# Kernel optimization log

Hardware: AMD Instinct MI355X
Metric: run time of the kernel (lower is better)

The kernel has to match this reference:

```python
import jax, jax.numpy as jnp
import numpy as np

EPS = 1e-5
PATCH_SIZES = [None, 13]
PATCH_WEIGHTS = [0.5, 0.5]


def _box(x, p):
    # sliding-window sum over spatial dims, VALID padding -> [B,C,H-p+1,W-p+1]
    return jax.lax.reduce_window(x, 0.0, jax.lax.add, (1, 1, p, p), (1, 1, 1, 1), 'VALID')


def _global_ncc(x1, x2):
    # InstanceNorm2d (biased var, eps) per (b,c) over spatial dims, then dot / (c*h*w)
    b, c, h, w = x1.shape
    m1 = jnp.mean(x1, axis=(2, 3), keepdims=True)
    m2 = jnp.mean(x2, axis=(2, 3), keepdims=True)
    v1 = jnp.mean((x1 - m1) ** 2, axis=(2, 3), keepdims=True)
    v2 = jnp.mean((x2 - m2) ** 2, axis=(2, 3), keepdims=True)
    n1 = (x1 - m1) * jax.lax.rsqrt(v1 + EPS)
    n2 = (x2 - m2) * jax.lax.rsqrt(v2 + EPS)
    return jnp.sum(n1 * n2, axis=(1, 2, 3)) / (c * h * w)


def _patch_ncc(x1, x2, p):
    # Equivalent fused form of: unfold -> rearrange (patch locations become
    # channels, pxp patch pixels become spatial) -> InstanceNorm2d -> dot.
    # Each pxp patch is normalized over its own pixels => local NCC.
    b, c, h, w = x1.shape
    n = p * p
    s1 = _box(x1, p)
    s2 = _box(x2, p)
    s11 = _box(x1 * x1, p)
    s22 = _box(x2 * x2, p)
    s12 = _box(x1 * x2, p)
    m1 = s1 / n
    m2 = s2 / n
    v1 = s11 / n - m1 * m1  # biased variance, matches InstanceNorm2d
    v2 = s22 / n - m2 * m2
    cross = s12 - n * m1 * m2  # sum_p (I-mI)(J-mJ)
    cc = cross * jax.lax.rsqrt((v1 + EPS) * (v2 + EPS))  # [B,C,H',W']
    hp, wp = h - p + 1, w - p + 1
    # original divides by (channels' * h' * w') where channels' = c*hp*wp, spatial = p*p
    return jnp.sum(cc, axis=(1, 2, 3)) / (c * hp * wp * n)


def setup_inputs() -> dict:
    key = jax.random.key(0)
    k1, k2 = jax.random.split(key)
    x1 = jax.random.normal(k1, (32, 1, 512, 512), dtype=jnp.float32)
    x2 = jax.random.normal(k2, (32, 1, 512, 512), dtype=jnp.float32)
    return {"x1": x1, "x2": x2}


def reference(x1, x2):
    scores = []
    for w, p in zip(PATCH_WEIGHTS, PATCH_SIZES):
        if p is None:
            scores.append(w * _global_ncc(x1, x2))
        else:
            scores.append(w * _patch_ncc(x1, x2, p))
    return jnp.stack(scores, axis=0).sum(axis=0)  # [B]
```

## Files before the change

kernel.cpp:

```cpp
#include <hip/hip_runtime.h>

#define EPS 1e-5f

typedef float v2f __attribute__((ext_vector_type(2)));

constexpr int B = 32;
constexpr int H = 512;
constexpr int W = 512;
constexpr int NPIX = H * W;
constexpr int P = 13;
constexpr int HP = H - P + 1;
constexpr int WP = W - P + 1;
constexpr int TILES_X = 4;
constexpr int BAND_OUT = 40;
constexpr int BANDS_Y = 13;
constexpr int G = 13;
constexpr int NGROUPS = 4;
constexpr int ITER_LAST_OWN = 20;
constexpr int ITER_LAST_EMIT = 32;
constexpr int BLOCKS_PER_B = TILES_X * BANDS_Y;
constexpr int RS = 140;

#define GLOAD_LDS16(gp, lp)                                                    \
  __builtin_amdgcn_global_load_lds(                                            \
      (const __attribute__((address_space(1))) unsigned int*)(const void*)(gp),\
      (__attribute__((address_space(3))) unsigned int*)(void*)(lp), 16, 0, 0)

__global__ __launch_bounds__(64) void ncc_fused_kernel(
    const float* __restrict__ x1, const float* __restrict__ x2,
    float* __restrict__ part) {
  const int bid = blockIdx.x;
  const int b    = bid / BLOCKS_PER_B;
  const int rem  = bid % BLOCKS_PER_B;
  const int tile = rem % TILES_X;
  const int band = rem / TILES_X;
  const bool last = (band == BANDS_Y - 1);
  const int x0 = tile * 128;
  const int y0 = last ? (HP - BAND_OUT) : band * BAND_OUT;
  const int tid = threadIdx.x;
  const int c0 = x0 + 2 * tid;
  const bool valid0 = c0 < WP;
  const bool valid1 = (c0 + 1) < WP;

  __shared__ float sa[2][G][RS];
  __shared__ float sb[2][G][RS];

  const float* r1 = x1 + (size_t)b * NPIX + (size_t)y0 * W + x0;
  const float* r2 = x2 + (size_t)b * NPIX + (size_t)y0 * W + x0;

  int qoff = tid * 4;
  { int mx = W - x0 - 4; if (qoff > mx) qoff = mx; }
  const bool loader = tid < 35;

  auto stage = [&](int g, int buf) {
    if (loader) {
#pragma unroll
      for (int r = 0; r < G; ++r) {
        GLOAD_LDS16(r1 + (size_t)(g * G + r) * W + qoff, &sa[buf][r][0]);
        GLOAD_LDS16(r2 + (size_t)(g * G + r) * W + qoff, &sb[buf][r][0]);
      }
    }
  };

  v2f rr1[G], rr2[G], rr11[G], rr22[G], rr12[G];
  v2f S1 = {0.f, 0.f}, S2 = {0.f, 0.f}, S11 = {0.f, 0.f}, S22 = {0.f, 0.f},
      S12 = {0.f, 0.f};
  v2f g1 = {0.f, 0.f}, g2 = {0.f, 0.f}, g11 = {0.f, 0.f}, g22 = {0.f, 0.f},
      g12 = {0.f, 0.f};
  float acc = 0.f;
  const float inv_n = 1.0f / 169.0f;

  auto step = [&](int u, int buf, int t, bool fill) {
    const float* pa = &sa[buf][u][2 * tid];
    const float* pb = &sb[buf][u][2 * tid];
    v2f A[7], Bv[7];
#pragma unroll
    for (int k = 0; k < 7; ++k) {
      A[k] = *(const v2f*)(pa + 2 * k);
      Bv[k] = *(const v2f*)(pb + 2 * k);
    }

    v2f q11 = A[0] * A[0], q22 = Bv[0] * Bv[0], q12 = A[0] * Bv[0];
    v2f h1v = A[0], h2v = Bv[0], h11v = q11, h22v = q22, h12v = q12;
#pragma unroll
    for (int k = 1; k < 6; ++k) {
      h1v += A[k];
      h2v += Bv[k];
      h11v += A[k] * A[k];
      h22v += Bv[k] * Bv[k];
      h12v += A[k] * Bv[k];
    }
    float a12 = A[6].x, b12 = Bv[6].x, a13 = A[6].y, b13 = Bv[6].y;
    float h1_0 = h1v.x + h1v.y + a12;
    float h2_0 = h2v.x + h2v.y + b12;
    float h11_0 = fmaf(a12, a12, h11v.x + h11v.y);
    float h22_0 = fmaf(b12, b12, h22v.x + h22v.y);
    float h12_0 = fmaf(a12, b12, h12v.x + h12v.y);
    v2f h1 = {h1_0, h1_0 - A[0].x + a13};
    v2f h2 = {h2_0, h2_0 - Bv[0].x + b13};
    v2f h11 = {h11_0, fmaf(a13, a13, h11_0 - q11.x)};
    v2f h22 = {h22_0, fmaf(b13, b13, h22_0 - q22.x)};
    v2f h12 = {h12_0, fmaf(a13, b13, h12_0 - q12.x)};

    bool owned = last ? (t >= ITER_LAST_OWN) : (t < BAND_OUT);
    if (owned) {
      g1 += A[0]; g2 += Bv[0]; g11 += q11; g22 += q22; g12 += q12;
    }

    if (fill) {
      S1 += h1; S2 += h2; S11 += h11; S22 += h22; S12 += h12;
    } else {
      S1 += h1 - rr1[u]; S2 += h2 - rr2[u];
      S11 += h11 - rr11[u]; S22 += h22 - rr22[u]; S12 += h12 - rr12[u];
    }
    rr1[u] = h1; rr2[u] = h2; rr11[u] = h11; rr22[u] = h22; rr12[u] = h12;

    bool do_out = (t >= 12) && (!last || t >= ITER_LAST_EMIT);
    if (do_out) {
      v2f m1 = S1 * inv_n, m2 = S2 * inv_n;
      v2f vv1 = S11 * inv_n - m1 * m1 + EPS;
      v2f vv2 = S22 * inv_n - m2 * m2 + EPS;
      v2f cross = S12 - (S1 * inv_n) * S2;
      v2f den = vv1 * vv2;
      float cc0 = cross.x * rsqrtf(den.x);
      float cc1 = cross.y * rsqrtf(den.y);
      acc += (valid0 ? cc0 : 0.f) + (valid1 ? cc1 : 0.f);
    }
  };

  stage(0, 0);
  __syncthreads();
  stage(1, 1);

#pragma unroll
  for (int u = 0; u < G; ++u) step(u, 0, u, true);
  __syncthreads();

#pragma clang loop unroll(disable)
  for (int g = 1; g < NGROUPS; ++g) {
    if (g + 1 < NGROUPS) stage(g + 1, (g + 1) & 1);
    const int buf = g & 1;
#pragma unroll
    for (int u = 0; u < G; ++u) step(u, buf, g * G + u, false);
    __syncthreads();
  }

  float v0 = acc;
  float w1 = g1.x + g1.y, w2 = g2.x + g2.y;
  float w3 = g11.x + g11.y, w4 = g22.x + g22.y, w5 = g12.x + g12.y;
#pragma unroll
  for (int off = 32; off > 0; off >>= 1) {
    v0 += __shfl_down(v0, off, 64);
    w1 += __shfl_down(w1, off, 64);
    w2 += __shfl_down(w2, off, 64);
    w3 += __shfl_down(w3, off, 64);
    w4 += __shfl_down(w4, off, 64);
    w5 += __shfl_down(w5, off, 64);
  }
  if (tid == 0) {
    float* o = part + (size_t)bid * 6;
    o[0] = v0; o[1] = w1; o[2] = w2; o[3] = w3; o[4] = w4; o[5] = w5;
  }
}

__global__ __launch_bounds__(64) void final_kernel(
    const float* __restrict__ part, float* __restrict__ out) {
  int b = blockIdx.x;
  int tid = threadIdx.x;
  float s[6] = {0.f, 0.f, 0.f, 0.f, 0.f, 0.f};
  for (int i = tid; i < BLOCKS_PER_B; i += 64) {
    const float* p = part + (size_t)(b * BLOCKS_PER_B + i) * 6;
#pragma unroll
    for (int k = 0; k < 6; ++k) s[k] += p[k];
  }
#pragma unroll
  for (int off = 32; off > 0; off >>= 1) {
#pragma unroll
    for (int k = 0; k < 6; ++k) s[k] += __shfl_down(s[k], off, 64);
  }
  if (tid == 0) {
    float Nf = (float)NPIX;
    float m1 = s[1] / Nf;
    float m2 = s[2] / Nf;
    float v1 = fmaf(-m1, m1, s[3] / Nf);
    float v2 = fmaf(-m2, m2, s[4] / Nf);
    float cross = fmaf(-Nf * m1, m2, s[5]);
    float g = cross * rsqrtf((v1 + EPS) * (v2 + EPS)) / Nf;
    float patch = s[0] / ((float)HP * (float)WP * 169.0f);
    out[b] = 0.5f * g + 0.5f * patch;
  }
}

extern "C" void kernel_launch(void* const* d_in, const int* in_sizes, int n_in,
                              void* d_out, int out_size, void* d_ws, size_t ws_size,
                              hipStream_t stream) {
  const float* x1 = (const float*)d_in[0];
  const float* x2 = (const float*)d_in[1];
  float* out = (float*)d_out;
  float* part = (float*)d_ws;

  ncc_fused_kernel<<<B * BLOCKS_PER_B, 64, 0, stream>>>(x1, x2, part);
  final_kernel<<<B, 64, 0, stream>>>(part, out);
}
```

Baseline: 122.3 us.

## Add fp16 conversion prepass with global stats; run patch kernel on fp16 inputs

```diff
diff --git a/kernel.cpp b/kernel.cpp
--- a/kernel.cpp
+++ b/kernel.cpp
@@ -3,6 +3,8 @@
 #define EPS 1e-5f
 
 typedef float v2f __attribute__((ext_vector_type(2)));
+typedef _Float16 h2 __attribute__((ext_vector_type(2)));
+typedef _Float16 h4 __attribute__((ext_vector_type(4)));
 
 constexpr int B = 32;
 constexpr int H = 512;
@@ -16,18 +18,63 @@
 constexpr int BANDS_Y = 13;
 constexpr int G = 13;
 constexpr int NGROUPS = 4;
-constexpr int ITER_LAST_OWN = 20;
 constexpr int ITER_LAST_EMIT = 32;
 constexpr int BLOCKS_PER_B = TILES_X * BANDS_Y;
-constexpr int RS = 140;
+constexpr int RSH = 144;
 
 #define GLOAD_LDS16(gp, lp)                                                    \
   __builtin_amdgcn_global_load_lds(                                            \
       (const __attribute__((address_space(1))) unsigned int*)(const void*)(gp),\
       (__attribute__((address_space(3))) unsigned int*)(void*)(lp), 16, 0, 0)
 
+__global__ __launch_bounds__(256) void prepass_kernel(
+    const float* __restrict__ x1, const float* __restrict__ x2,
+    _Float16* __restrict__ p1, _Float16* __restrict__ p2,
+    float* __restrict__ gs) {
+  int b = blockIdx.x >> 5;
+  int chunk = blockIdx.x & 31;
+  int tid = threadIdx.x;
+  size_t base4 = (size_t)b * (NPIX / 4) + (size_t)chunk * 2048;
+  const float4* q1 = (const float4*)x1 + base4;
+  const float4* q2 = (const float4*)x2 + base4;
+  h4* o1 = (h4*)p1 + base4;
+  h4* o2 = (h4*)p2 + base4;
+
+  float s1 = 0.f, s2 = 0.f, s11 = 0.f, s22 = 0.f, s12 = 0.f;
+#pragma unroll
+  for (int i = 0; i < 8; ++i) {
+    float4 a = q1[i * 256 + tid];
+    float4 c = q2[i * 256 + tid];
+    s1 += a.x + a.y + a.z + a.w;
+    s2 += c.x + c.y + c.z + c.w;
+    s11 = fmaf(a.x, a.x, fmaf(a.y, a.y, fmaf(a.z, a.z, fmaf(a.w, a.w, s11))));
+    s22 = fmaf(c.x, c.x, fmaf(c.y, c.y, fmaf(c.z, c.z, fmaf(c.w, c.w, s22))));
+    s12 = fmaf(a.x, c.x, fmaf(a.y, c.y, fmaf(a.z, c.z, fmaf(a.w, c.w, s12))));
+    h4 ha = {(_Float16)a.x, (_Float16)a.y, (_Float16)a.z, (_Float16)a.w};
+    h4 hc = {(_Float16)c.x, (_Float16)c.y, (_Float16)c.z, (_Float16)c.w};
+    o1[i * 256 + tid] = ha;
+    o2[i * 256 + tid] = hc;
+  }
+
+  float v[5] = {s1, s2, s11, s22, s12};
+  __shared__ float red[5][4];
+#pragma unroll
+  for (int k = 0; k < 5; ++k)
+#pragma unroll
+    for (int off = 32; off > 0; off >>= 1) v[k] += __shfl_down(v[k], off, 64);
+  int lane = tid & 63, wave = tid >> 6;
+  if (lane == 0)
+#pragma unroll
+    for (int k = 0; k < 5; ++k) red[k][wave] = v[k];
+  __syncthreads();
+  if (tid == 0)
+#pragma unroll
+    for (int k = 0; k < 5; ++k)
+      atomicAdd(&gs[k * B + b], red[k][0] + red[k][1] + red[k][2] + red[k][3]);
+}
+
 __global__ __launch_bounds__(64) void ncc_fused_kernel(
-    const float* __restrict__ x1, const float* __restrict__ x2,
+    const _Float16* __restrict__ p1, const _Float16* __restrict__ p2,
     float* __restrict__ part) {
   const int bid = blockIdx.x;
   const int b    = bid / BLOCKS_PER_B;
@@ -42,15 +89,15 @@
   const bool valid0 = c0 < WP;
   const bool valid1 = (c0 + 1) < WP;
 
-  __shared__ float sa[2][G][RS];
-  __shared__ float sb[2][G][RS];
-
-  const float* r1 = x1 + (size_t)b * NPIX + (size_t)y0 * W + x0;
-  const float* r2 = x2 + (size_t)b * NPIX + (size_t)y0 * W + x0;
-
-  int qoff = tid * 4;
-  { int mx = W - x0 - 4; if (qoff > mx) qoff = mx; }
-  const bool loader = tid < 35;
+  __shared__ _Float16 sa[2][G][RSH];
+  __shared__ _Float16 sb[2][G][RSH];
+
+  const _Float16* r1 = p1 + (size_t)b * NPIX + (size_t)y0 * W + x0;
+  const _Float16* r2 = p2 + (size_t)b * NPIX + (size_t)y0 * W + x0;
+
+  int qoff = tid * 8;
+  { int mx = W - x0 - 8; if (qoff > mx) qoff = mx; }
+  const bool loader = tid < 18;
 
   auto stage = [&](int g, int buf) {
     if (loader) {
@@ -65,19 +112,19 @@
   v2f rr1[G], rr2[G], rr11[G], rr22[G], rr12[G];
   v2f S1 = {0.f, 0.f}, S2 = {0.f, 0.f}, S11 = {0.f, 0.f}, S22 = {0.f, 0.f},
       S12 = {0.f, 0.f};
-  v2f g1 = {0.f, 0.f}, g2 = {0.f, 0.f}, g11 = {0.f, 0.f}, g22 = {0.f, 0.f},
-      g12 = {0.f, 0.f};
   float acc = 0.f;
   const float inv_n = 1.0f / 169.0f;
 
   auto step = [&](int u, int buf, int t, bool fill) {
-    const float* pa = &sa[buf][u][2 * tid];
-    const float* pb = &sb[buf][u][2 * tid];
+    const h2* pa = (const h2*)&sa[buf][u][0];
+    const h2* pb = (const h2*)&sb[buf][u][0];
     v2f A[7], Bv[7];
 #pragma unroll
     for (int k = 0; k < 7; ++k) {
-      A[k] = *(const v2f*)(pa + 2 * k);
-      Bv[k] = *(const v2f*)(pb + 2 * k);
+      h2 xa = pa[tid + k];
+      h2 xb = pb[tid + k];
+      A[k].x = (float)xa.x;  A[k].y = (float)xa.y;
+      Bv[k].x = (float)xb.x; Bv[k].y = (float)xb.y;
     }
 
     v2f q11 = A[0] * A[0], q22 = Bv[0] * Bv[0], q12 = A[0] * Bv[0];
@@ -102,11 +149,6 @@
     v2f h22 = {h22_0, fmaf(b13, b13, h22_0 - q22.x)};
     v2f h12 = {h12_0, fmaf(a13, b13, h12_0 - q12.x)};
 
-    bool owned = last ? (t >= ITER_LAST_OWN) : (t < BAND_OUT);
-    if (owned) {
-      g1 += A[0]; g2 += Bv[0]; g11 += q11; g22 += q22; g12 += q12;
-    }
-
     if (fill) {
       S1 += h1; S2 += h2; S11 += h11; S22 += h22; S12 += h12;
     } else {
@@ -145,48 +187,29 @@
     __syncthreads();
   }
 
-  float v0 = acc;
-  float w1 = g1.x + g1.y, w2 = g2.x + g2.y;
-  float w3 = g11.x + g11.y, w4 = g22.x + g22.y, w5 = g12.x + g12.y;
-#pragma unroll
-  for (int off = 32; off > 0; off >>= 1) {
-    v0 += __shfl_down(v0, off, 64);
-    w1 += __shfl_down(w1, off, 64);
-    w2 += __shfl_down(w2, off, 64);
-    w3 += __shfl_down(w3, off, 64);
-    w4 += __shfl_down(w4, off, 64);
-    w5 += __shfl_down(w5, off, 64);
-  }
-  if (tid == 0) {
-    float* o = part + (size_t)bid * 6;
-    o[0] = v0; o[1] = w1; o[2] = w2; o[3] = w3; o[4] = w4; o[5] = w5;
-  }
+#pragma unroll
+  for (int off = 32; off > 0; off >>= 1) acc += __shfl_down(acc, off, 64);
+  if (tid == 0) part[bid] = acc;
 }
 
 __global__ __launch_bounds__(64) void final_kernel(
-    const float* __restrict__ part, float* __restrict__ out) {
+    const float* __restrict__ part, const float* __restrict__ gs,
+    float* __restrict__ out) {
   int b = blockIdx.x;
   int tid = threadIdx.x;
-  float s[6] = {0.f, 0.f, 0.f, 0.f, 0.f, 0.f};
-  for (int i = tid; i < BLOCKS_PER_B; i += 64) {
-    const float* p = part + (size_t)(b * BLOCKS_PER_B + i) * 6;
-#pragma unroll
-    for (int k = 0; k < 6; ++k) s[k] += p[k];
-  }
-#pragma unroll
-  for (int off = 32; off > 0; off >>= 1) {
-#pragma unroll
-    for (int k = 0; k < 6; ++k) s[k] += __shfl_down(s[k], off, 64);
-  }
+  float s = 0.f;
+  if (tid < BLOCKS_PER_B) s = part[b * BLOCKS_PER_B + tid];
+#pragma unroll
+  for (int off = 32; off > 0; off >>= 1) s += __shfl_down(s, off, 64);
   if (tid == 0) {
     float Nf = (float)NPIX;
-    float m1 = s[1] / Nf;
-    float m2 = s[2] / Nf;
-    float v1 = fmaf(-m1, m1, s[3] / Nf);
-    float v2 = fmaf(-m2, m2, s[4] / Nf);
-    float cross = fmaf(-Nf * m1, m2, s[5]);
+    float m1 = gs[0 * B + b] / Nf;
+    float m2 = gs[1 * B + b] / Nf;
+    float v1 = fmaf(-m1, m1, gs[2 * B + b] / Nf);
+    float v2 = fmaf(-m2, m2, gs[3 * B + b] / Nf);
+    float cross = fmaf(-Nf * m1, m2, gs[4 * B + b]);
     float g = cross * rsqrtf((v1 + EPS) * (v2 + EPS)) / Nf;
-    float patch = s[0] / ((float)HP * (float)WP * 169.0f);
+    float patch = s / ((float)HP * (float)WP * 169.0f);
     out[b] = 0.5f * g + 0.5f * patch;
   }
 }
@@ -197,8 +220,13 @@
   const float* x1 = (const float*)d_in[0];
   const float* x2 = (const float*)d_in[1];
   float* out = (float*)d_out;
-  float* part = (float*)d_ws;
-
-  ncc_fused_kernel<<<B * BLOCKS_PER_B, 64, 0, stream>>>(x1, x2, part);
-  final_kernel<<<B, 64, 0, stream>>>(part, out);
-}
+  _Float16* p1 = (_Float16*)d_ws;
+  _Float16* p2 = p1 + (size_t)B * NPIX;
+  float* gs = (float*)(p2 + (size_t)B * NPIX);
+  float* part = gs + 5 * B;
+
+  hipMemsetAsync(gs, 0, 5 * B * sizeof(float), stream);
+  prepass_kernel<<<B * 32, 256, 0, stream>>>(x1, x2, p1, p2, gs);
+  ncc_fused_kernel<<<B * BLOCKS_PER_B, 64, 0, stream>>>(p1, p2, part);
+  final_kernel<<<B, 64, 0, stream>>>(part, gs, out);
+}
```

Result: slower. 137.0 us (+12.0%).
